# Performance work log

Hardware: AMD Instinct MI355X
Metric: run time of the kernel (lower is better)

## Reference

```python
import jax, jax.numpy as jnp
import numpy as np

N = 8192      # num nodes (fea.shape[0])
IN = 512      # in_features (fea.shape[1])
H = 64        # nhidden
DEG = 32      # avg degree
E = N * DEG   # num edges


def setup_inputs() -> dict:
    key = jax.random.key(0)
    k1, k2, k3 = jax.random.split(key, 3)
    x = jax.random.normal(k1, (N, IN), dtype=jnp.float32)
    # glorot-uniform-scaled params (stored as [in, out] for x @ W)
    W = jax.random.uniform(k2, (IN, H), jnp.float32, -1.0, 1.0) * np.sqrt(6.0 / (IN + H))
    a = jax.random.uniform(k3, (2 * H, 1), jnp.float32, -1.0, 1.0) * np.sqrt(6.0 / (2 * H + 1))
    # structured edge list: no self-loops, no duplicate edges (matches nonzero of a
    # zero-diagonal adjacency; indexed-assignment scatter then has unique targets)
    src = jnp.repeat(jnp.arange(N, dtype=jnp.int32), DEG)
    offs = jnp.tile(jnp.arange(1, DEG + 1, dtype=jnp.int32), N)
    dst = (src + offs) % N
    edge_index = jnp.stack([src, dst])  # [2, E]
    return {"x": x, "W": W, "a": a, "edge_index": edge_index}


def reference(x, W, a, edge_index):
    src, dst = edge_index[0], edge_index[1]
    n = x.shape[0]
    h = a.shape[0] // 2
    Wx = x @ W                                   # [N, H]
    # cat(fea1, fea2) @ a  ==  fea1 @ a[:h] + fea2 @ a[h:]
    e = (Wx @ a[:h])[src, 0] + (Wx @ a[h:])[dst, 0]   # [E]
    coef = jnp.exp(jax.nn.leaky_relu(e, negative_slope=0.1))
    # dense scatter into NxN adjacency (faithful to original)
    A = jnp.zeros((n, n), dtype=x.dtype).at[src, dst].set(coef)
    s1 = A.sum(axis=1)
    # rows with zero sum get a 1 on the diagonal (diag is 0 there, so add == set)
    diag = jnp.arange(n)
    A = A.at[diag, diag].add(jnp.where(s1 == 0, jnp.float32(1.0), jnp.float32(0.0)))
    # (A.t() / A.sum(1)).t()  ==  row-normalize
    return A / A.sum(axis=1, keepdims=True)
```

## Files before the change

kernel.cpp:

```cpp
#include <hip/hip_runtime.h>

#define N_NODES 8192
#define IN_F    512
#define NH      64
#define RB      512

typedef float v4f __attribute__((ext_vector_type(4)));

__global__ void k_prep(const float* __restrict__ W, const float* __restrict__ a,
                       float* __restrict__ wa1, float* __restrict__ wa2) {
    int tid = blockIdx.x * blockDim.x + threadIdx.x;
    if (tid < IN_F) {
        const float* wrow = W + tid * NH;
        float d1 = 0.f, d2 = 0.f;
#pragma unroll
        for (int k = 0; k < NH; ++k) {
            float w = wrow[k];
            d1 += w * a[k];
            d2 += w * a[NH + k];
        }
        wa1[tid] = d1;
        wa2[tid] = d2;
    }
}

__global__ void k_scores(const float* __restrict__ x, const float* __restrict__ wa1,
                         const float* __restrict__ wa2, float* __restrict__ s1,
                         float* __restrict__ s2) {
    int gid  = blockIdx.x * blockDim.x + threadIdx.x;
    int node = gid >> 6;
    int lane = threadIdx.x & 63;
    if (node >= N_NODES) return;
    const float4* xr = (const float4*)(x + (size_t)node * IN_F);
    const float4* w1 = (const float4*)wa1;
    const float4* w2 = (const float4*)wa2;
    float d1 = 0.f, d2 = 0.f;
#pragma unroll
    for (int i = 0; i < 2; ++i) {
        int idx = lane + 64 * i;
        float4 xv = xr[idx];
        float4 a1 = w1[idx];
        float4 a2 = w2[idx];
        d1 += xv.x * a1.x + xv.y * a1.y + xv.z * a1.z + xv.w * a1.w;
        d2 += xv.x * a2.x + xv.y * a2.y + xv.z * a2.z + xv.w * a2.w;
    }
#pragma unroll
    for (int off = 32; off > 0; off >>= 1) {
        d1 += __shfl_xor(d1, off, 64);
        d2 += __shfl_xor(d2, off, 64);
    }
    if (lane == 0) { s1[node] = d1; s2[node] = d2; }
}

__global__ __launch_bounds__(RB)
void k_row(const int* __restrict__ src, const int* __restrict__ dst,
           const float* __restrict__ s1, const float* __restrict__ s2,
           float* __restrict__ out, int deg) {
    const int row = blockIdx.x;
    const int tid = threadIdx.x;
    __shared__ float rowbuf[N_NODES];
    __shared__ float inv_s;

    int sv = row, dv = -1;
    const bool edge_lane = (tid < deg);
    if (edge_lane) {
        int e = row * deg + tid;
        sv = src[e];
        dv = dst[e];
    }

    v4f* rb4 = (v4f*)rowbuf;
    const v4f z = {0.f, 0.f, 0.f, 0.f};
#pragma unroll
    for (int i = 0; i < (N_NODES / 4) / RB; ++i)
        rb4[tid + RB * i] = z;
    __syncthreads();

    if (tid < 64) {
        float c = 0.f;
        if (edge_lane) {
            float ev = s1[sv] + s2[dv];
            float l  = ev > 0.f ? ev : 0.1f * ev;
            c = expf(l);
            if (sv == row) rowbuf[dv] = c;
        }
        float t = c;
#pragma unroll
        for (int off = 32; off > 0; off >>= 1)
            t += __shfl_xor(t, off, 64);
        if (tid == 0) {
            if (t == 0.f) { rowbuf[row] = 1.0f; inv_s = 1.0f; }
            else          { inv_s = 1.0f / t; }
        }
    }
    __syncthreads();
    const float inv = inv_s;

    v4f* orow4 = (v4f*)(out + (size_t)row * N_NODES);
#pragma unroll
    for (int i = 0; i < (N_NODES / 4) / RB; ++i) {
        int idx = tid + RB * i;
        v4f v = rb4[idx];
        v *= inv;
        __builtin_nontemporal_store(v, &orow4[idx]);
    }
}

extern "C" void kernel_launch(void* const* d_in, const int* in_sizes, int n_in,
                              void* d_out, int out_size, void* d_ws, size_t ws_size,
                              hipStream_t stream) {
    const float* x  = (const float*)d_in[0];
    const float* W  = (const float*)d_in[1];
    const float* a  = (const float*)d_in[2];
    const int*   ei = (const int*)d_in[3];
    const int E = in_sizes[3] / 2;
    const int deg = E / N_NODES;
    const int* src = ei;
    const int* dst = ei + E;

    float* ws  = (float*)d_ws;
    float* wa1 = ws;
    float* wa2 = wa1 + IN_F;
    float* s1  = wa2 + IN_F;
    float* s2  = s1 + N_NODES;

    float* out = (float*)d_out;

    k_prep<<<(IN_F + 255) / 256, 256, 0, stream>>>(W, a, wa1, wa2);
    k_scores<<<(N_NODES * 64) / 256, 256, 0, stream>>>(x, wa1, wa2, s1, s2);
    k_row<<<N_NODES, RB, 0, stream>>>(src, dst, s1, s2, out, deg);
}
```

Before: 287.1 us.

## Specialize row kernel for circulant edge pattern with runtime check and fallback

```diff
diff --git a/kernel.cpp b/kernel.cpp
--- a/kernel.cpp
+++ b/kernel.cpp
@@ -3,13 +3,15 @@
 #define N_NODES 8192
 #define IN_F    512
 #define NH      64
-#define RB      512
+#define RB      256
 
 typedef float v4f __attribute__((ext_vector_type(4)));
 
 __global__ void k_prep(const float* __restrict__ W, const float* __restrict__ a,
-                       float* __restrict__ wa1, float* __restrict__ wa2) {
+                       float* __restrict__ wa1, float* __restrict__ wa2,
+                       int* __restrict__ flag) {
     int tid = blockIdx.x * blockDim.x + threadIdx.x;
+    if (tid == 0) flag[0] = 1;
     if (tid < IN_F) {
         const float* wrow = W + tid * NH;
         float d1 = 0.f, d2 = 0.f;
@@ -21,6 +23,21 @@
         }
         wa1[tid] = d1;
         wa2[tid] = d2;
+    }
+}
+
+__global__ void k_check(const int* __restrict__ src, const int* __restrict__ dst,
+                        int* __restrict__ flag, int E, int deg) {
+    int e = blockIdx.x * blockDim.x + threadIdx.x;
+    bool ok = true;
+    if (e < E) {
+        int r = e / deg, j = e - r * deg;
+        int dexp = r + 1 + j;
+        if (dexp >= N_NODES) dexp -= N_NODES;
+        ok = (src[e] == r) && (dst[e] == dexp);
+    }
+    if (__ballot(!ok) != 0ull) {
+        if ((threadIdx.x & 63) == 0) atomicAnd(flag, 0);
     }
 }
 
@@ -55,54 +72,70 @@
 __global__ __launch_bounds__(RB)
 void k_row(const int* __restrict__ src, const int* __restrict__ dst,
            const float* __restrict__ s1, const float* __restrict__ s2,
-           float* __restrict__ out, int deg) {
+           const int* __restrict__ flag, float* __restrict__ out, int deg) {
     const int row = blockIdx.x;
     const int tid = threadIdx.x;
-    __shared__ float rowbuf[N_NODES];
-    __shared__ float inv_s;
-
-    int sv = row, dv = -1;
-    const bool edge_lane = (tid < deg);
-    if (edge_lane) {
-        int e = row * deg + tid;
-        sv = src[e];
-        dv = dst[e];
-    }
-
-    v4f* rb4 = (v4f*)rowbuf;
-    const v4f z = {0.f, 0.f, 0.f, 0.f};
-#pragma unroll
-    for (int i = 0; i < (N_NODES / 4) / RB; ++i)
-        rb4[tid + RB * i] = z;
-    __syncthreads();
+    __shared__ float ncoefs[64];
+    __shared__ int   cols[64];
+    __shared__ float diag_s;
 
     if (tid < 64) {
-        float c = 0.f;
-        if (edge_lane) {
-            float ev = s1[sv] + s2[dv];
-            float l  = ev > 0.f ? ev : 0.1f * ev;
-            c = expf(l);
-            if (sv == row) rowbuf[dv] = c;
+        float c = 0.f; int col = -1;
+        if (tid < deg) {
+            int e  = row * deg + tid;
+            int sv = src[e], dv = dst[e];
+            if (sv == row) {
+                float ev = s1[sv] + s2[dv];
+                float l  = ev > 0.f ? ev : 0.1f * ev;
+                c = expf(l);
+                col = dv;
+            }
         }
         float t = c;
 #pragma unroll
         for (int off = 32; off > 0; off >>= 1)
             t += __shfl_xor(t, off, 64);
-        if (tid == 0) {
-            if (t == 0.f) { rowbuf[row] = 1.0f; inv_s = 1.0f; }
-            else          { inv_s = 1.0f / t; }
-        }
+        float inv = (t == 0.f) ? 1.f : 1.f / t;
+        ncoefs[tid] = c * inv;
+        cols[tid]   = col;
+        if (tid == 0) diag_s = (t == 0.f) ? 1.f : 0.f;
     }
     __syncthreads();
-    const float inv = inv_s;
 
-    v4f* orow4 = (v4f*)(out + (size_t)row * N_NODES);
+    const float dg = diag_s;
+    float* orf   = out + (size_t)row * N_NODES;
+    v4f*   orow4 = (v4f*)orf;
+    const v4f z = {0.f, 0.f, 0.f, 0.f};
+
+    if (flag[0] != 0) {
 #pragma unroll
-    for (int i = 0; i < (N_NODES / 4) / RB; ++i) {
-        int idx = tid + RB * i;
-        v4f v = rb4[idx];
-        v *= inv;
-        __builtin_nontemporal_store(v, &orow4[idx]);
+        for (int k = 0; k < (N_NODES / 4) / RB; ++k) {
+            int slot = tid + RB * k;
+            int ob = (slot << 2) - row - 1;
+            if (ob < 0) ob += N_NODES;
+            v4f v = z;
+            if (ob < deg || ob >= N_NODES - 4) {
+#pragma unroll
+                for (int m = 0; m < 4; ++m) {
+                    int off = ob + m;
+                    if (off >= N_NODES) off -= N_NODES;
+                    float val = 0.f;
+                    if (off < deg) val = ncoefs[off];
+                    else if (off == N_NODES - 1) val = dg;
+                    v[m] = val;
+                }
+            }
+            __builtin_nontemporal_store(v, &orow4[slot]);
+        }
+    } else {
+#pragma unroll
+        for (int k = 0; k < (N_NODES / 4) / RB; ++k)
+            __builtin_nontemporal_store(z, &orow4[tid + RB * k]);
+        __syncthreads();
+        if (tid < 64) {
+            if (cols[tid] >= 0) orf[cols[tid]] = ncoefs[tid];
+            if (tid == 0 && dg != 0.f) orf[row] = 1.f;
+        }
     }
 }
 
@@ -118,15 +151,17 @@
     const int* src = ei;
     const int* dst = ei + E;
 
-    float* ws  = (float*)d_ws;
-    float* wa1 = ws;
-    float* wa2 = wa1 + IN_F;
-    float* s1  = wa2 + IN_F;
-    float* s2  = s1 + N_NODES;
+    float* ws   = (float*)d_ws;
+    float* wa1  = ws;
+    float* wa2  = wa1 + IN_F;
+    float* s1   = wa2 + IN_F;
+    float* s2   = s1 + N_NODES;
+    int*   flag = (int*)(s2 + N_NODES);
 
     float* out = (float*)d_out;
 
-    k_prep<<<(IN_F + 255) / 256, 256, 0, stream>>>(W, a, wa1, wa2);
+    k_prep<<<(IN_F + 255) / 256, 256, 0, stream>>>(W, a, wa1, wa2, flag);
+    k_check<<<(E + 255) / 256, 256, 0, stream>>>(src, dst, flag, E, deg);
     k_scores<<<(N_NODES * 64) / 256, 256, 0, stream>>>(x, wa1, wa2, s1, s2);
-    k_row<<<N_NODES, RB, 0, stream>>>(src, dst, s1, s2, out, deg);
+    k_row<<<N_NODES, RB, 0, stream>>>(src, dst, s1, s2, flag, out, deg);
 }
```

New measurement: 289.9 us. About the same (+1.0%).
